# Optimization experiments

Measured on AMD Instinct MI355X. Metric: run time of the kernel, lower is better.

## Reference

```python
import jax, jax.numpy as jnp
from jax import lax
import numpy as np

HH = WW = 128          # backbone feature map (2048px image / stride 16)
C_IN = 512
FEAT_STRIDE = 16
N_ANCHOR = 9
NMS_THRESH = 0.7
N_PRE_NMS = 6000
N_POST_NMS = 300
MIN_SIZE = 16
NEG = jnp.float32(-1e30)


def _anchor_base(base_size=16, ratios=(0.5, 1.0, 2.0), scales=(8, 16, 32)):
    py = px = base_size / 2.0
    ab = np.zeros((len(ratios) * len(scales), 4), np.float32)
    for i, r in enumerate(ratios):
        for j, s in enumerate(scales):
            h = base_size * s * np.sqrt(r)
            w = base_size * s * np.sqrt(1.0 / r)
            ab[i * len(scales) + j] = [py - h / 2, px - w / 2, py + h / 2, px + w / 2]
    return ab


def _shifted_anchors(hh, ww):
    # (y1, x1, y2, x2) anchors enumerated row-major over (y, x), anchors innermost
    ab = _anchor_base()
    sy = np.arange(0, hh * FEAT_STRIDE, FEAT_STRIDE, dtype=np.float32)
    sx = np.arange(0, ww * FEAT_STRIDE, FEAT_STRIDE, dtype=np.float32)
    sx, sy = np.meshgrid(sx, sy)
    shift = np.stack((sy.ravel(), sx.ravel(), sy.ravel(), sx.ravel()), axis=1)
    anc = (ab[None, :, :] + shift[:, None, :]).reshape(-1, 4)
    return jnp.asarray(anc)


def _conv(x, w, b):
    y = lax.conv_general_dilated(x, w, (1, 1), 'SAME',
                                 dimension_numbers=('NHWC', 'HWIO', 'NHWC'))
    return y + b


def _loc2bbox(anchor, loc):
    sh = anchor[:, 2] - anchor[:, 0]
    sw = anchor[:, 3] - anchor[:, 1]
    scy = anchor[:, 0] + 0.5 * sh
    scx = anchor[:, 1] + 0.5 * sw
    cy = loc[:, 0] * sh + scy
    cx = loc[:, 1] * sw + scx
    h = jnp.exp(loc[:, 2]) * sh
    w = jnp.exp(loc[:, 3]) * sw
    return jnp.stack([cy - 0.5 * h, cx - 0.5 * w, cy + 0.5 * h, cx + 0.5 * w], axis=1)


def _nms(boxes, scores, thresh, n_out):
    # Greedy NMS with a fixed output size; invalid slots are zeroed.
    y1, x1, y2, x2 = boxes[:, 0], boxes[:, 1], boxes[:, 2], boxes[:, 3]
    areas = (y2 - y1) * (x2 - x1)

    def step(valid, _):
        s = jnp.where(valid, scores, NEG)
        i = jnp.argmax(s)
        ok = s[i] > NEG
        iy1 = jnp.maximum(y1, y1[i]); ix1 = jnp.maximum(x1, x1[i])
        iy2 = jnp.minimum(y2, y2[i]); ix2 = jnp.minimum(x2, x2[i])
        inter = jnp.maximum(iy2 - iy1, 0.0) * jnp.maximum(ix2 - ix1, 0.0)
        iou = inter / (areas + areas[i] - inter + 1e-9)
        valid = valid & (iou <= thresh)  # picked box suppresses itself (iou=1)
        return valid, (i, ok)

    _, (idx, oks) = lax.scan(step, jnp.ones(scores.shape, bool), None, length=n_out)
    return boxes[idx] * oks[:, None].astype(boxes.dtype)


def _proposals(loc, fg_score, anchor, img_h, img_w, scale):
    dst = _loc2bbox(anchor, loc)
    dst = jnp.stack([jnp.clip(dst[:, 0], 0.0, img_h),
                     jnp.clip(dst[:, 1], 0.0, img_w),
                     jnp.clip(dst[:, 2], 0.0, img_h),
                     jnp.clip(dst[:, 3], 0.0, img_w)], axis=1)
    min_size = MIN_SIZE * scale
    hs = dst[:, 2] - dst[:, 0]
    ws = dst[:, 3] - dst[:, 1]
    keep = (hs >= min_size) & (ws >= min_size)
    sc = jnp.where(keep, fg_score, -jnp.inf)
    top_s, top_i = lax.top_k(sc, N_PRE_NMS)
    return _nms(dst[top_i], top_s, NMS_THRESH, N_POST_NMS)


def _rpn_forward(x, conv_w, conv_b, loc_w, loc_b, score_w, score_b, img_h, img_w, scale):
    n, hh, ww, _ = x.shape
    anchor = _shifted_anchors(hh, ww)                    # [hh*ww*9, 4]
    h = jax.nn.relu(_conv(x, conv_w, conv_b))            # [n, hh, ww, 512]
    rpn_loc = _conv(h, loc_w, loc_b).reshape(n, -1, 4)   # [n, hh*ww*9, 4]
    rpn_score_map = _conv(h, score_w, score_b)           # [n, hh, ww, 18]
    soft = jax.nn.softmax(rpn_score_map.reshape(n, hh, ww, N_ANCHOR, 2), axis=-1)
    rpn_fg = soft[..., 1].reshape(n, -1)                 # [n, hh*ww*9]
    rpn_score = rpn_score_map.reshape(n, -1, 2)
    roi = _proposals(rpn_loc[0], rpn_fg[0], anchor, img_h, img_w, scale)  # [300, 4]
    return rpn_loc, rpn_score, roi, anchor


def setup_inputs() -> dict:
    key = jax.random.key(0)
    ks = jax.random.split(key, 4)
    return {
        "x": jax.random.normal(ks[0], (1, HH, WW, C_IN), jnp.float32),
        "conv_w": jax.random.normal(ks[1], (3, 3, C_IN, 512), jnp.float32) * 0.02,
        "conv_b": jnp.zeros((512,), jnp.float32),
        "loc_w": jax.random.normal(ks[2], (1, 1, 512, 36), jnp.float32) * 0.02,
        "loc_b": jnp.zeros((36,), jnp.float32),
        "score_w": jax.random.normal(ks[3], (1, 1, 512, 18), jnp.float32) * 0.02,
        "score_b": jnp.zeros((18,), jnp.float32),
        "img_h": HH * FEAT_STRIDE,
        "img_w": WW * FEAT_STRIDE,
        "scale": 1,
    }


def reference(x, conv_w, conv_b, loc_w, loc_b, score_w, score_b, img_h, img_w, scale):
    return _rpn_forward(x, conv_w, conv_b, loc_w, loc_b, score_w, score_b,
                        float(img_h), float(img_w), float(scale))
```

## Files before the change

kernel.cpp:

```cpp
#include <hip/hip_runtime.h>
#include <math.h>

typedef unsigned int u32;
typedef unsigned long long u64;
typedef _Float16 half8 __attribute__((ext_vector_type(8)));
typedef float f32x4 __attribute__((ext_vector_type(4)));
typedef float f32x16 __attribute__((ext_vector_type(16)));

#define N_PIX 16384
#define N_ANC 147456
#define N_PRE 6000
#define TIE_BASE 6144
#define TIE_CAP  16384

#define OFF_H      0ULL
#define OFF_BOXES  33554432ULL
#define OFF_KEYS   35913728ULL
#define OFF_W54    36503552ULL
#define OFF_B54    36634624ULL
#define OFF_HIST1  36634880ULL
#define OFF_HIST2  36897024ULL
#define OFF_CTRL   37159168ULL
#define OFF_CAND   37159424ULL
#define OFF_SBOX   37339648ULL
#define OFF_MASK   37437952ULL
#define BASE_NEEDED 41961984ULL
#define OFF_XH     41961984ULL
#define OFF_XL     58739200ULL
#define OFF_WHT    75516416ULL
#define OFF_WLT    80235008ULL
#define FULL_NEEDED 84953600ULL

#define KEY_NEGINF 0x007FFFFFu

#define MASK_BYTES 4524032ULL

struct AB { float v[36]; };


__device__ __forceinline__ void d_init_body(int i0, u32* hist1, u32* hist2, u32* ctrl, float* roi,
                       float* w54, float* b54,
                       const float* __restrict__ loc_w, const float* __restrict__ loc_b,
                       const float* __restrict__ score_w, const float* __restrict__ score_b) {
  const int stride = 256 * 256;
  const int TOT = 65536 * 2 + 64 + 1200 + 32768 + 64;
  for (int i = i0; i < TOT; i += stride) {
    if (i < 65536) hist1[i] = 0u;
    else if (i < 131072) hist2[i - 65536] = 0u;
    else if (i < 131136) ctrl[i - 131072] = 0u;
    else if (i < 132336) roi[i - 131136] = 0.f;
    else if (i < 165104) {
      int j = i - 132336;
      int k = j >> 6, oc = j & 63;
      float v = 0.f;
      if (oc < 36) v = loc_w[k * 36 + oc];
      else if (oc < 54) v = score_w[k * 18 + oc - 36];
      w54[(((k >> 2) << 6) + oc) * 4 + (k & 3)] = v;
    } else {
      int oc = i - 165104;
      float v = 0.f;
      if (oc < 36) v = loc_b[oc];
      else if (oc < 54) v = score_b[oc - 36];
      b54[oc] = v;
    }
  }
}

__device__ __forceinline__ void d_split_x_body(int b, int t, const float* __restrict__ x,
                                               _Float16* __restrict__ xh, _Float16* __restrict__ xl) {
  const int gid = b * 256 + t;
  const int base = gid << 3;
  float a[8];
  *(float4*)&a[0] = *(const float4*)(x + base);
  *(float4*)&a[4] = *(const float4*)(x + base + 4);
  half8 hh, ll;
#pragma unroll
  for (int j = 0; j < 8; ++j) {
    _Float16 hi = (_Float16)a[j];
    hh[j] = hi;
    ll[j] = (_Float16)((a[j] - (float)hi) * 2048.0f);
  }
  *(half8*)(xh + base) = hh;
  *(half8*)(xl + base) = ll;
}

__device__ __forceinline__ void d_split_w_body(int kb, int cb, int t, const float* __restrict__ w,
                                               _Float16* __restrict__ whT, _Float16* __restrict__ wlT,
                                               _Float16 (*th)[72], _Float16 (*tl)[72]) {
  {
    const int r = t >> 2, cq = t & 3;
    float a[16];
    const float* wp = w + ((size_t)(kb * 64 + r) << 9) + cb * 64 + cq * 16;
#pragma unroll
    for (int j = 0; j < 4; ++j) *(float4*)&a[j << 2] = *(const float4*)(wp + (j << 2));
    half8 h0, h1, l0, l1;
#pragma unroll
    for (int j = 0; j < 8; ++j) {
      _Float16 hi = (_Float16)a[j];
      h0[j] = hi; l0[j] = (_Float16)((a[j] - (float)hi) * 2048.0f);
    }
#pragma unroll
    for (int j = 0; j < 8; ++j) {
      _Float16 hi = (_Float16)a[8 + j];
      h1[j] = hi; l1[j] = (_Float16)((a[8 + j] - (float)hi) * 2048.0f);
    }
    *(half8*)&th[r][cq * 16]     = h0;
    *(half8*)&th[r][cq * 16 + 8] = h1;
    *(half8*)&tl[r][cq * 16]     = l0;
    *(half8*)&tl[r][cq * 16 + 8] = l1;
  }
  __syncthreads();
  {
    const int c = t >> 2, kq = t & 3;
    half8 o0, o1, p0, p1;
#pragma unroll
    for (int j = 0; j < 8; ++j) { o0[j] = th[kq * 16 + j][c];     p0[j] = tl[kq * 16 + j][c]; }
#pragma unroll
    for (int j = 0; j < 8; ++j) { o1[j] = th[kq * 16 + 8 + j][c]; p1[j] = tl[kq * 16 + 8 + j][c]; }
    const size_t dst = (size_t)(cb * 64 + c) * 4608 + kb * 64 + kq * 16;
    *(half8*)(whT + dst)     = o0;
    *(half8*)(whT + dst + 8) = o1;
    *(half8*)(wlT + dst)     = p0;
    *(half8*)(wlT + dst + 8) = p1;
  }
}

__global__ void k_init(u32* hist1, u32* hist2, u32* ctrl, float* roi,
                       float* w54, float* b54,
                       const float* __restrict__ loc_w, const float* __restrict__ loc_b,
                       const float* __restrict__ score_w, const float* __restrict__ score_b) {
  const int i0 = blockIdx.x * blockDim.x + threadIdx.x;
  d_init_body(i0, hist1, hist2, ctrl, roi, w54, b54, loc_w, loc_b, score_w, score_b);
}

__global__ __launch_bounds__(256) void k_prep(const float* __restrict__ x,
                                              _Float16* __restrict__ xh, _Float16* __restrict__ xl,
                                              const float* __restrict__ w,
                                              _Float16* __restrict__ whT, _Float16* __restrict__ wlT,
                                              u32* hist1, u32* hist2, u32* ctrl, float* roi,
                                              float* w54, float* b54,
                                              const float* __restrict__ loc_w, const float* __restrict__ loc_b,
                                              const float* __restrict__ score_w, const float* __restrict__ score_b) {
  __shared__ _Float16 th[64][72];
  __shared__ _Float16 tl[64][72];
  const int b = blockIdx.x;
  const int t = threadIdx.x;
  if (b < 4096) {
    d_split_x_body(b, t, x, xh, xl);
  } else if (b < 4672) {
    const int idx = b - 4096;
    d_split_w_body(idx % 72, idx / 72, t, w, whT, wlT, th, tl);
  } else {
    d_init_body((b - 4672) * 256 + t, hist1, hist2, ctrl, roi, w54, b54, loc_w, loc_b, score_w, score_b);
  }
}

__global__ __launch_bounds__(256, 2) void k_conv_pre(const _Float16* __restrict__ xh,
                                                     const _Float16* __restrict__ xl,
                                                     const _Float16* __restrict__ whT,
                                                     const _Float16* __restrict__ wlT,
                                                     const float* __restrict__ bias,
                                                     float* __restrict__ h) {
  __shared__ _Float16 As[2][2][4][128][8];
  __shared__ _Float16 Bs[2][2][4][128][8];

  const int bid = blockIdx.x;
  const int q   = bid >> 3;
  const int nb  = q >> 4;
  const int y   = ((bid & 7) << 4) + (q & 15);

  const int t  = threadIdx.x;
  const int wv = t >> 6, lane = t & 63;
  const int m0 = (wv >> 1) << 6;
  const int n0 = (wv & 1) << 6;
  const int ln5 = lane & 31;
  const int kh  = lane >> 5;

  const int s_m = t >> 1;
  const int kq0 = (t & 1) << 1;
  const int ch0 = kq0 << 3;

  f32x16 acc_hh[2][2];
  f32x16 acc_x[2][2];
#pragma unroll
  for (int i = 0; i < 2; ++i)
#pragma unroll
    for (int j = 0; j < 2; ++j) { acc_hh[i][j] = (f32x16)0.f; acc_x[i][j] = (f32x16)0.f; }

  const int ct0 = (s_m - 1) << 9;
  const int ct1 = s_m << 9;
  const int ct2 = (s_m + 1) << 9;
  const bool cok0 = (s_m >= 1);
  const bool cok2 = (s_m <= 126);
  const u32 bb = (u32)(nb * 128 + s_m) * 4608u + (u32)ch0;

  half8 rah0, rah1, ral0, ral1, rbh0, rbh1, rbl0, rbl1;

#define CONV_LOAD(KB)                                                            \
  {                                                                              \
    const int ci_   = (KB) / 9;                           \
    const int tap_  = (KB) - ci_ * 9;                        \
    const int ky_   = tap_ / 3, kx_ = tap_ - ky_ * 3;                            \
    const int cin0_ = ci_ << 5;                                                  \
    const int yy_   = y + ky_ - 1;                                               \
    const bool rok_ = (yy_ >= 0) && (yy_ < 128);                                 \
    const int colterm_ = (kx_ == 0) ? ct0 : ((kx_ == 1) ? ct1 : ct2);            \
    const bool cok_    = (kx_ == 0) ? cok0 : ((kx_ == 1) ? true : cok2);         \
    if (rok_ && cok_) {                                                          \
      const u32 aoff_ = (u32)((yy_ << 16) + cin0_ + ch0 + colterm_);             \
      rah0 = *(const half8*)(xh + aoff_);                                        \
      rah1 = *(const half8*)(xh + aoff_ + 8);                                    \
      ral0 = *(const half8*)(xl + aoff_);                                        \
      ral1 = *(const half8*)(xl + aoff_ + 8);                                    \
    } else {                                                                     \
      rah0 = (half8)(_Float16)0; rah1 = (half8)(_Float16)0;                      \
      ral0 = (half8)(_Float16)0; ral1 = (half8)(_Float16)0;                      \
    }                                                                            \
    const u32 boff_ = bb + (u32)(tap_ * 512 + cin0_);                            \
    rbh0 = *(const half8*)(whT + boff_);                                         \
    rbh1 = *(const half8*)(whT + boff_ + 8);                                     \
    rbl0 = *(const half8*)(wlT + boff_);                                         \
    rbl1 = *(const half8*)(wlT + boff_ + 8);                                     \
  }

#define CONV_STORE(BUF)                                                          \
  {                                                                              \
    *(half8*)As[BUF][0][kq0][s_m]     = rah0;                                    \
    *(half8*)As[BUF][0][kq0 + 1][s_m] = rah1;                                    \
    *(half8*)As[BUF][1][kq0][s_m]     = ral0;                                    \
    *(half8*)As[BUF][1][kq0 + 1][s_m] = ral1;                                    \
    *(half8*)Bs[BUF][0][kq0][s_m]     = rbh0;                                    \
    *(half8*)Bs[BUF][0][kq0 + 1][s_m] = rbh1;                                    \
    *(half8*)Bs[BUF][1][kq0][s_m]     = rbl0;                                    \
    *(half8*)Bs[BUF][1][kq0 + 1][s_m] = rbl1;                                    \
  }

#define FRAGS(KS, AH, AL, BH, BL)                                                \
  {                                                                              \
    const int kq_ = ((KS) << 1) + kh;                                            \
    _Pragma("unroll")                                                            \
    for (int i = 0; i < 2; ++i) {                                                \
      AH[i] = *(const half8*)As[cur][0][kq_][m0 + (i << 5) + ln5];               \
      AL[i] = *(const half8*)As[cur][1][kq_][m0 + (i << 5) + ln5];               \
      BH[i] = *(const half8*)Bs[cur][0][kq_][n0 + (i << 5) + ln5];               \
      BL[i] = *(const half8*)Bs[cur][1][kq_][n0 + (i << 5) + ln5];               \
    }                                                                            \
  }

#define MFMA12(AH, AL, BH, BL)                                                   \
  {                                                                              \
    _Pragma("unroll")                                                            \
    for (int mi = 0; mi < 2; ++mi)                                               \
      _Pragma("unroll")                                                          \
      for (int ni = 0; ni < 2; ++ni) {                                           \
        acc_hh[mi][ni] = __builtin_amdgcn_mfma_f32_32x32x16_f16(AH[mi], BH[ni], acc_hh[mi][ni], 0, 0, 0); \
        acc_x[mi][ni]  = __builtin_amdgcn_mfma_f32_32x32x16_f16(AH[mi], BL[ni], acc_x[mi][ni], 0, 0, 0);  \
        acc_x[mi][ni]  = __builtin_amdgcn_mfma_f32_32x32x16_f16(AL[mi], BH[ni], acc_x[mi][ni], 0, 0, 0);  \
      }                                                                          \
  }

  CONV_LOAD(0);
  CONV_STORE(0);
  __syncthreads();

  int cur = 0;
#pragma unroll 1
  for (int kb = 0; kb < 143; ++kb) {
    half8 a0h[2], a0l[2], b0h[2], b0l[2];
    FRAGS(0, a0h, a0l, b0h, b0l);
    CONV_LOAD(kb + 1);
    __builtin_amdgcn_sched_barrier(0);
    __builtin_amdgcn_s_setprio(1);
    MFMA12(a0h, a0l, b0h, b0l);
    __builtin_amdgcn_s_setprio(0);
    half8 a1h[2], a1l[2], b1h[2], b1l[2];
    FRAGS(1, a1h, a1l, b1h, b1l);
    __builtin_amdgcn_s_setprio(1);
    MFMA12(a1h, a1l, b1h, b1l);
    __builtin_amdgcn_s_setprio(0);
    CONV_STORE(cur ^ 1);
    __syncthreads();
    cur ^= 1;
  }
  {
    half8 a0h[2], a0l[2], b0h[2], b0l[2];
    FRAGS(0, a0h, a0l, b0h, b0l);
    MFMA12(a0h, a0l, b0h, b0l);
    half8 a1h[2], a1l[2], b1h[2], b1l[2];
    FRAGS(1, a1h, a1l, b1h, b1l);
    MFMA12(a1h, a1l, b1h, b1l);
  }
#undef CONV_LOAD
#undef CONV_STORE
#undef FRAGS
#undef MFMA12

  const float inv2048 = 1.0f / 2048.0f;
#pragma unroll
  for (int mi = 0; mi < 2; ++mi)
#pragma unroll
    for (int ni = 0; ni < 2; ++ni) {
      const int col = n0 + (ni << 5) + ln5;
      const float bbv = bias[(nb << 7) + col];
#pragma unroll
      for (int r = 0; r < 16; ++r) {
        const int row = m0 + (mi << 5) + (r & 3) + ((r >> 2) << 3) + (kh << 2);
        float v = acc_hh[mi][ni][r] + acc_x[mi][ni][r] * inv2048 + bbv;
        h[(((size_t)((y << 7) + row)) << 9) + (nb << 7) + col] = fmaxf(v, 0.f);
      }
    }
}

#define APAD 40
__global__ __launch_bounds__(256, 2) void k_conv_fb(const float* __restrict__ x,
                                                    const float* __restrict__ w,
                                                    const float* __restrict__ bias,
                                                    float* __restrict__ h) {
  __shared__ _Float16 Ah[128][APAD];
  __shared__ _Float16 Al[128][APAD];
  __shared__ _Float16 Bh[128][APAD];
  __shared__ _Float16 Bl[128][APAD];

  const int y  = blockIdx.x;
  const int nb = blockIdx.y;
  const int t  = threadIdx.x;
  const int wv = t >> 6, lane = t & 63;
  const int m0 = (wv >> 1) << 6;
  const int n0 = (wv & 1) << 6;
  const int fm = lane & 15;
  const int fq = lane >> 4;
  const int sa_m = t >> 1;
  const int sa_h = (t & 1) << 4;
  const int sb_n = t & 127;
  const int sb_kg = (t >> 7) << 4;

  f32x4 acc_hh[4][4];
  f32x4 acc_x[4][4];
#pragma unroll
  for (int i = 0; i < 4; ++i)
#pragma unroll
    for (int j = 0; j < 4; ++j) { acc_hh[i][j] = (f32x4)0.f; acc_x[i][j] = (f32x4)0.f; }

#pragma unroll 1
  for (int kb = 0; kb < 144; ++kb) {
    const int tap  = kb >> 4;
    const int ky   = tap / 3, kx = tap - ky * 3;
    const int cin0 = (kb & 15) << 5;
    {
      const int yy = y + ky - 1;
      const int xx = sa_m + kx - 1;
      float av[16];
      if (yy >= 0 && yy < 128 && xx >= 0 && xx < 128) {
        const float* ap = x + (((size_t)((yy << 7) + xx)) << 9) + cin0 + sa_h;
#pragma unroll
        for (int j = 0; j < 4; ++j) *(float4*)&av[j << 2] = *(const float4*)(ap + (j << 2));
      } else {
#pragma unroll
        for (int j = 0; j < 16; ++j) av[j] = 0.f;
      }
      half8 h0, h1, l0, l1;
#pragma unroll
      for (int j = 0; j < 8; ++j) {
        _Float16 hi = (_Float16)av[j];
        h0[j] = hi; l0[j] = (_Float16)((av[j] - (float)hi) * 2048.0f);
      }
#pragma unroll
      for (int j = 0; j < 8; ++j) {
        _Float16 hi = (_Float16)av[8 + j];
        h1[j] = hi; l1[j] = (_Float16)((av[8 + j] - (float)hi) * 2048.0f);
      }
      *(half8*)&Ah[sa_m][sa_h]     = h0;
      *(half8*)&Ah[sa_m][sa_h + 8] = h1;
      *(half8*)&Al[sa_m][sa_h]     = l0;
      *(half8*)&Al[sa_m][sa_h + 8] = l1;
    }
    {
      const float* bp = w + ((size_t)(tap * 512 + cin0 + sb_kg) << 9) + (nb << 7) + sb_n;
      float bv[16];
#pragma unroll
      for (int j = 0; j < 16; ++j) bv[j] = bp[(size_t)j << 9];
      half8 h0, h1, l0, l1;
#pragma unroll
      for (int j = 0; j < 8; ++j) {
        _Float16 hi = (_Float16)bv[j];
        h0[j] = hi; l0[j] = (_Float16)((bv[j] - (float)hi) * 2048.0f);
      }
#pragma unroll
      for (int j = 0; j < 8; ++j) {
        _Float16 hi = (_Float16)bv[8 + j];
        h1[j] = hi; l1[j] = (_Float16)((bv[8 + j] - (float)hi) * 2048.0f);
      }
      *(half8*)&Bh[sb_n][sb_kg]     = h0;
      *(half8*)&Bh[sb_n][sb_kg + 8] = h1;
      *(half8*)&Bl[sb_n][sb_kg]     = l0;
      *(half8*)&Bl[sb_n][sb_kg + 8] = l1;
    }
    __syncthreads();
    half8 ah[4], al[4], bh[4], bl[4];
#pragma unroll
    for (int i = 0; i < 4; ++i) {
      ah[i] = *(const half8*)&Ah[m0 + (i << 4) + fm][fq << 3];
      al[i] = *(const half8*)&Al[m0 + (i << 4) + fm][fq << 3];
      bh[i] = *(const half8*)&Bh[n0 + (i << 4) + fm][fq << 3];
      bl[i] = *(const half8*)&Bl[n0 + (i << 4) + fm][fq << 3];
    }
#pragma unroll
    for (int mi = 0; mi < 4; ++mi)
#pragma unroll
      for (int ni = 0; ni < 4; ++ni) {
        acc_hh[mi][ni] = __builtin_amdgcn_mfma_f32_16x16x32_f16(ah[mi], bh[ni], acc_hh[mi][ni], 0, 0, 0);
        acc_x[mi][ni]  = __builtin_amdgcn_mfma_f32_16x16x32_f16(ah[mi], bl[ni], acc_x[mi][ni], 0, 0, 0);
        acc_x[mi][ni]  = __builtin_amdgcn_mfma_f32_16x16x32_f16(al[mi], bh[ni], acc_x[mi][ni], 0, 0, 0);
      }
    __syncthreads();
  }
  const float inv2048 = 1.0f / 2048.0f;
#pragma unroll
  for (int mi = 0; mi < 4; ++mi)
#pragma unroll
    for (int ni = 0; ni < 4; ++ni) {
      const int col = n0 + (ni << 4) + fm;
      const float bb = bias[(nb << 7) + col];
#pragma unroll
      for (int r = 0; r < 4; ++r) {
        const int row = m0 + (mi << 4) + (fq << 2) + r;
        float v = acc_hh[mi][ni][r] + acc_x[mi][ni][r] * inv2048 + bb;
        h[(((size_t)((y << 7) + row)) << 9) + (nb << 7) + col] = fmaxf(v, 0.f);
      }
    }
}

__global__ __launch_bounds__(256) void k_heads(const float* __restrict__ h,
        const float4* __restrict__ w54, const float* __restrict__ b54,
        float* __restrict__ out0, float* __restrict__ out1, float* __restrict__ out3,
        float4* __restrict__ boxes, u32* __restrict__ keys, u32* __restrict__ hist1,
        const int* __restrict__ p_ih, const int* __restrict__ p_iw,
        const int* __restrict__ p_sc, AB ab) {
  __shared__ float hl[16 * 512];
  __shared__ float vals[16][64];
  const int t = threadIdx.x;
  const int wv = t >> 6, lane = t & 63;
  const int pbase = blockIdx.x << 4;

#pragma unroll
  for (int j = 0; j < 8; ++j) {
    const int f = (j << 8) + t;
    ((float4*)hl)[f] = ((const float4*)(h + ((size_t)pbase << 9)))[f];
  }
  __syncthreads();

  const float* hp = hl + ((wv << 2) << 9);
  float a0 = 0.f, a1 = 0.f, a2 = 0.f, a3 = 0.f;
#pragma unroll 4
  for (int kq = 0; kq < 128; ++kq) {
    const float4 wvv = w54[(kq << 6) + lane];
    const float4 h0 = *(const float4*)(hp + (kq << 2));
    const float4 h1 = *(const float4*)(hp + 512 + (kq << 2));
    const float4 h2 = *(const float4*)(hp + 1024 + (kq << 2));
    const float4 h3 = *(const float4*)(hp + 1536 + (kq << 2));
    a0 += h0.x * wvv.x + h0.y * wvv.y + h0.z * wvv.z + h0.w * wvv.w;
    a1 += h1.x * wvv.x + h1.y * wvv.y + h1.z * wvv.z + h1.w * wvv.w;
    a2 += h2.x * wvv.x + h2.y * wvv.y + h2.z * wvv.z + h2.w * wvv.w;
    a3 += h3.x * wvv.x + h3.y * wvv.y + h3.z * wvv.z + h3.w * wvv.w;
  }
  const float bb = b54[lane];
  float av[4] = {a0 + bb, a1 + bb, a2 + bb, a3 + bb};
#pragma unroll
  for (int px = 0; px < 4; ++px) {
    const int p = pbase + (wv << 2) + px;
    vals[(wv << 2) + px][lane] = av[px];
    if (lane < 36) out0[p * 36 + lane] = av[px];
    else if (lane < 54) out1[p * 18 + lane - 36] = av[px];
  }
  __syncthreads();

  if (lane < 36) {
    const int px = lane / 9, a = lane - px * 9;
    const int p = pbase + (wv << 2) + px;
    const float* vv = vals[(wv << 2) + px];
    const float l0 = vv[(a << 2) + 0], l1 = vv[(a << 2) + 1];
    const float l2 = vv[(a << 2) + 2], l3 = vv[(a << 2) + 3];
    const float s0 = vv[36 + (a << 1)], s1 = vv[37 + (a << 1)];
    const int yq = p >> 7, xq = p & 127;
    const float fy = (float)(yq << 4), fx = (float)(xq << 4);
    const float ay1 = ab.v[(a << 2) + 0] + fy;
    const float ax1 = ab.v[(a << 2) + 1] + fx;
    const float ay2 = ab.v[(a << 2) + 2] + fy;
    const float ax2 = ab.v[(a << 2) + 3] + fx;
    const int idx = p * 9 + a;
    *(float4*)(out3 + ((size_t)idx << 2)) = make_float4(ay1, ax1, ay2, ax2);

    const float sh = ay2 - ay1, sw = ax2 - ax1;
    const float scy = ay1 + 0.5f * sh, scx = ax1 + 0.5f * sw;
    const float cy = l0 * sh + scy, cx = l1 * sw + scx;
    const float bh = expf(l2) * sh, bw = expf(l3) * sw;
    const float IH = (float)p_ih[0], IW = (float)p_iw[0];
    float d0 = fminf(fmaxf(cy - 0.5f * bh, 0.f), IH);
    float d1 = fminf(fmaxf(cx - 0.5f * bw, 0.f), IW);
    float d2 = fminf(fmaxf(cy + 0.5f * bh, 0.f), IH);
    float d3 = fminf(fmaxf(cx + 0.5f * bw, 0.f), IW);
    boxes[idx] = make_float4(d0, d1, d2, d3);

    const float minsz = 16.f * (float)p_sc[0];
    const bool keep = (d2 - d0 >= minsz) && (d3 - d1 >= minsz);
    const float mx = fmaxf(s0, s1);
    const float e0 = expf(s0 - mx), e1 = expf(s1 - mx);
    const float fg = e1 / (e0 + e1);
    const float sc = keep ? fg : -INFINITY;
    const u32 u = __float_as_uint(sc);
    const u32 key = (u & 0x80000000u) ? ~u : (u | 0x80000000u);
    keys[idx] = key;
    atomicAdd(&hist1[key >> 16], 1u);
  }
}

__global__ void k_hist2(const u32* __restrict__ keys, const u32* __restrict__ ctrl,
                        u32* __restrict__ hist2) {
  const u32 b1 = ctrl[0];
  int i = blockIdx.x * blockDim.x + threadIdx.x;
  if (i < N_ANC) {
    const u32 k = keys[i];
    if ((k >> 16) == b1) atomicAdd(&hist2[k & 0xFFFFu], 1u);
  }
}

__global__ __launch_bounds__(1024) void k_findcut(const u32* __restrict__ hist,
                                                  u32* __restrict__ ctrl, int mode) {
  __shared__ u32 csum[1024];
  __shared__ u32 suf[1024];
  const int t = threadIdx.x;
  const u32 target = (mode == 0) ? (u32)N_PRE : ((u32)N_PRE - ctrl[1]);
  const int base = t << 6;
  u32 s = 0;
  for (int i = 0; i < 64; ++i) s += hist[base + i];
  csum[t] = s;
  suf[t] = s;
  __syncthreads();
  for (int off = 1; off < 1024; off <<= 1) {
    u32 add = (t + off < 1024) ? suf[t + off] : 0u;
    __syncthreads();
    suf[t] += add;
    __syncthreads();
  }
  const u32 excl = suf[t] - csum[t];
  if (excl < target && target <= suf[t]) {
    u32 cum = excl;
    int bkt = base;
    for (int i = 63; i >= 0; --i) {
      const u32 hh = hist[base + i];
      if (cum < target && target <= cum + hh) { bkt = base + i; break; }
      cum += hh;
    }
    if (mode == 0) { ctrl[0] = (u32)bkt; ctrl[1] = cum; }
    else {
      const u32 Kstar = (ctrl[0] << 16) | (u32)bkt;
      const u32 A = ctrl[1] + cum;
      u32 need = (u32)N_PRE - A;
      if (Kstar == KEY_NEGINF) need = 0u;
      ctrl[2] = Kstar; ctrl[3] = A; ctrl[4] = need;
      ctrl[7] = A + need;
    }
  }
}

__global__ void k_compact(const u32* __restrict__ keys, u32* __restrict__ ctrl,
                          u64* __restrict__ cand) {
  const u32 Kstar = ctrl[2];
  const u32 need  = ctrl[4];
  int i = blockIdx.x * blockDim.x + threadIdx.x;
  if (i >= N_ANC) return;
  const u32 k = keys[i];
  if (k > Kstar) {
    const u32 pos = atomicAdd(&ctrl[5], 1u);
    cand[pos] = ((u64)k << 32) | (u64)(u32)(~(u32)i);
  } else if (k == Kstar && need != 0u) {
    const u32 pos = atomicAdd(&ctrl[6], 1u);
    if (pos < (u32)TIE_CAP) cand[TIE_BASE + pos] = ((u64)Kstar << 32) | (u64)(u32)(~(u32)i);
  }
}

__global__ __launch_bounds__(128) void k_rank(const u32* __restrict__ ctrl,
                                              const u64* __restrict__ cand,
                                              const float4* __restrict__ boxes,
                                              float4* __restrict__ sbox) {
  __shared__ u32 wred[2];
  const u32 A   = ctrl[3];
  const u32 tcc = min(ctrl[6], (u32)TIE_CAP);
  const u32 C   = A + tcc;
  const u32 L   = ctrl[7];
  const int t   = threadIdx.x;
  for (u32 i = blockIdx.x; i < C; i += gridDim.x) {
    const u64 v = (i < A) ? cand[i] : cand[TIE_BASE + (i - A)];
    u32 cnt = 0;
    for (u32 j = t; j < A; j += 128) cnt += (cand[j] > v);
    for (u32 j = t; j < tcc; j += 128) cnt += (cand[TIE_BASE + j] > v);
#pragma unroll
    for (int off = 32; off > 0; off >>= 1) cnt += __shfl_xor(cnt, off);
    if ((t & 63) == 0) wred[t >> 6] = cnt;
    __syncthreads();
    if (t == 0) {
      const u32 rank = wred[0] + wred[1];
      if (rank < L) {
        const u32 idx = ~((u32)(v & 0xFFFFFFFFULL));
        sbox[rank] = boxes[idx];
      }
    }
    __syncthreads();
  }
}

__global__ __launch_bounds__(256) void k_mask(const u32* __restrict__ ctrl,
                                              const float4* __restrict__ sbox,
                                              u64* __restrict__ mask) {
  const int L = (int)ctrl[7];
  const int rb = blockIdx.y;
  if (rb * 64 >= L) return;
  const int wv = threadIdx.x >> 6;
  const int lane = threadIdx.x & 63;
  const int cw = (blockIdx.x << 2) + wv;
  if (cw > 93 || cw < rb) return;
  const int j = cw * 64 + lane;
  const bool jok = (j < L);
  const float4 cb = jok ? sbox[j] : make_float4(0.f, 0.f, 0.f, 0.f);
  const float careaJ = (cb.z - cb.x) * (cb.w - cb.y);
  const int rbase = rb * 64;
  const float4 rbx = (rbase + lane < L) ? sbox[rbase + lane] : make_float4(0.f, 0.f, 0.f, 0.f);
  const int rmax = min(64, L - rbase);
  for (int r = 0; r < rmax; ++r) {
    const float ry1 = __shfl(rbx.x, r), rx1 = __shfl(rbx.y, r);
    const float ry2 = __shfl(rbx.z, r), rx2 = __shfl(rbx.w, r);
    const float ra = (ry2 - ry1) * (rx2 - rx1);
    const float iy1 = fmaxf(cb.x, ry1), ix1 = fmaxf(cb.y, rx1);
    const float iy2 = fminf(cb.z, ry2), ix2 = fminf(cb.w, rx2);
    const float inter = fmaxf(iy2 - iy1, 0.f) * fmaxf(ix2 - ix1, 0.f);
    const float iou = inter / (careaJ + ra - inter + 1e-9f);
    const bool bit = jok && (iou > 0.7f);
    const u64 bal = __ballot(bit);
    if (lane == 0) mask[(size_t)(rbase + r) * 94 + cw] = bal;
  }
}

__device__ inline u64 valid_mask_fn(int base, int L) {
  const int r = L - base;
  if (r <= 0) return 0ULL;
  if (r >= 64) return ~0ULL;
  return (1ULL << r) - 1ULL;
}
__device__ inline u64 above_mask_fn(int base, int i) {
  if (i < base) return ~0ULL;
  const int s = i - base + 1;
  if (s >= 64) return 0ULL;
  return (~0ULL) << s;
}

__device__ __forceinline__ void gload_lds16(const void* g, void* l) {
  __builtin_amdgcn_global_load_lds(
      (const __attribute__((address_space(1))) void*)g,
      (__attribute__((address_space(3))) void*)l, 16, 0, 0);
}

__global__ __launch_bounds__(64) void k_greedy(const u32* __restrict__ ctrl,
                                               const float* __restrict__ sboxf,
                                               const u64* __restrict__ mask,
                                               float* __restrict__ roi) {
  __shared__ char lds[4 * 12288];
  const int lane = threadIdx.x;
  const int L = (int)ctrl[7];
  if (L <= 0) return;
  const char* gmask = (const char*)mask;
  const char* gend  = gmask + MASK_BYTES;
  const int nbatch = (L + 15) >> 4;

#define GISSUE(BB)                                                         \
  {                                                                        \
    const char* gb_ = gmask + (size_t)(BB) * 12032;                        \
    char* lb_ = lds + ((BB) & 3) * 12288;                                  \
    _Pragma("unroll")                                                      \
    for (int j_ = 0; j_ < 12; ++j_) {                                      \
      const char* ga_ = gb_ + j_ * 1024;                                   \
      if (ga_ + 1024 > gend) ga_ = gend - 1024;    \
      gload_lds16(ga_ + lane * 16, lb_ + j_ * 1024);                       \
    }                                                                      \
  }

  int issued = 0;
  for (; issued < nbatch && issued < 4; ++issued) GISSUE(issued);

  const int base0 = lane << 6;
  const int base1 = (64 + lane) << 6;
  const u64 v0 = valid_mask_fn(base0, L);
  const u64 v1 = (lane < 30) ? valid_mask_fn(base1, L) : 0ULL;
  u64 rem0 = 0ULL, rem1 = 0ULL;
  int i = 0, kept = 0;

  for (int b = 0; b < nbatch && i >= 0 && kept < 300; ++b) {
    const int out = issued - b - 1;
    if (out >= 3)      asm volatile("s_waitcnt vmcnt(36)" ::: "memory");
    else if (out == 2) asm volatile("s_waitcnt vmcnt(24)" ::: "memory");
    else if (out == 1) asm volatile("s_waitcnt vmcnt(12)" ::: "memory");
    else               asm volatile("s_waitcnt vmcnt(0)"  ::: "memory");
    const int hi = (b + 1) << 4;
    while (i >= 0 && i < hi && kept < 300) {
      if (lane < 4) roi[kept * 4 + lane] = sboxf[(size_t)i * 4 + lane];
      ++kept;
      const u64* rowp = (const u64*)(lds + (((u32)i >> 4) & 3) * 12288 + (i & 15) * 752);
      rem0 |= rowp[lane];
      if (lane < 30) rem1 |= rowp[64 + lane];
      const u64 f0 = ~rem0 & v0 & above_mask_fn(base0, i);
      const u64 f1 = ~rem1 & v1 & above_mask_fn(base1, i);
      int c0 = f0 ? (base0 + (int)__builtin_ctzll(f0)) : 0x7FFFFFFF;
      int c1 = f1 ? (base1 + (int)__builtin_ctzll(f1)) : 0x7FFFFFFF;
      int c = min(c0, c1);
#pragma unroll
      for (int off = 1; off < 64; off <<= 1) c = min(c, __shfl_xor(c, off));
      i = (c == 0x7FFFFFFF) ? -1 : c;
    }
    if (issued < nbatch) { GISSUE(issued); ++issued; }
  }
#undef GISSUE
}

extern "C" void kernel_launch(void* const* d_in, const int* in_sizes, int n_in,
                              void* d_out, int out_size, void* d_ws, size_t ws_size,
                              hipStream_t stream) {
  (void)in_sizes; (void)n_in; (void)out_size;
  if (ws_size < BASE_NEEDED) return;
  const bool fast = (ws_size >= FULL_NEEDED);

  const float* x       = (const float*)d_in[0];
  const float* conv_w  = (const float*)d_in[1];
  const float* conv_b  = (const float*)d_in[2];
  const float* loc_w   = (const float*)d_in[3];
  const float* loc_b   = (const float*)d_in[4];
  const float* score_w = (const float*)d_in[5];
  const float* score_b = (const float*)d_in[6];
  const int* p_ih = (const int*)d_in[7];
  const int* p_iw = (const int*)d_in[8];
  const int* p_sc = (const int*)d_in[9];

  float* out0 = (float*)d_out;
  float* out1 = out0 + 589824;
  float* roi  = out1 + 294912;
  float* out3 = roi + 1200;

  char* ws = (char*)d_ws;
  float*     h     = (float*)(ws + OFF_H);
  float4*    boxes = (float4*)(ws + OFF_BOXES);
  u32*       keys  = (u32*)(ws + OFF_KEYS);
  float*     w54   = (float*)(ws + OFF_W54);
  float*     b54   = (float*)(ws + OFF_B54);
  u32*       hist1 = (u32*)(ws + OFF_HIST1);
  u32*       hist2 = (u32*)(ws + OFF_HIST2);
  u32*       ctrl  = (u32*)(ws + OFF_CTRL);
  u64*       cand  = (u64*)(ws + OFF_CAND);
  float4*    sbox  = (float4*)(ws + OFF_SBOX);
  u64*       mask  = (u64*)(ws + OFF_MASK);
  _Float16*  xh    = (_Float16*)(ws + OFF_XH);
  _Float16*  xl    = (_Float16*)(ws + OFF_XL);
  _Float16*  whT   = (_Float16*)(ws + OFF_WHT);
  _Float16*  wlT   = (_Float16*)(ws + OFF_WLT);

  AB ab;
  {
    const double ratios[3] = {0.5, 1.0, 2.0};
    const double scales[3] = {8.0, 16.0, 32.0};
    for (int i = 0; i < 3; ++i)
      for (int j = 0; j < 3; ++j) {
        const double hh = 16.0 * scales[j] * sqrt(ratios[i]);
        const double wwv = 16.0 * scales[j] * sqrt(1.0 / ratios[i]);
        const int a = i * 3 + j;
        ab.v[a * 4 + 0] = (float)(8.0 - hh / 2.0);
        ab.v[a * 4 + 1] = (float)(8.0 - wwv / 2.0);
        ab.v[a * 4 + 2] = (float)(8.0 + hh / 2.0);
        ab.v[a * 4 + 3] = (float)(8.0 + wwv / 2.0);
      }
  }

  if (fast) {
    hipLaunchKernelGGL(k_prep, dim3(4928), dim3(256), 0, stream,
                       x, xh, xl, conv_w, whT, wlT,
                       hist1, hist2, ctrl, roi, w54, b54, loc_w, loc_b, score_w, score_b);
    hipLaunchKernelGGL(k_conv_pre, dim3(512), dim3(256), 0, stream, xh, xl, whT, wlT, conv_b, h);
  } else {
    hipLaunchKernelGGL(k_init, dim3(256), dim3(256), 0, stream,
                       hist1, hist2, ctrl, roi, w54, b54, loc_w, loc_b, score_w, score_b);
    hipLaunchKernelGGL(k_conv_fb, dim3(128, 4), dim3(256), 0, stream, x, conv_w, conv_b, h);
  }
  hipLaunchKernelGGL(k_heads, dim3(1024), dim3(256), 0, stream,
                     h, (const float4*)w54, b54, out0, out1, out3, boxes, keys, hist1,
                     p_ih, p_iw, p_sc, ab);
  hipLaunchKernelGGL(k_findcut, dim3(1), dim3(1024), 0, stream, hist1, ctrl, 0);
  hipLaunchKernelGGL(k_hist2, dim3(576), dim3(256), 0, stream, keys, ctrl, hist2);
  hipLaunchKernelGGL(k_findcut, dim3(1), dim3(1024), 0, stream, hist2, ctrl, 1);
  hipLaunchKernelGGL(k_compact, dim3(576), dim3(256), 0, stream, keys, ctrl, cand);
  hipLaunchKernelGGL(k_rank, dim3(8192), dim3(128), 0, stream, ctrl, cand, boxes, sbox);
  hipLaunchKernelGGL(k_mask, dim3(24, 94), dim3(256), 0, stream, ctrl, sbox, mask);
  hipLaunchKernelGGL(k_greedy, dim3(1), dim3(64), 0, stream, ctrl, (const float*)sbox, mask, roi);
}
```

Before: 717.6 us.

## Load conv weights directly into registers and skip NMS batches via ballot search

The conv GEMM no longer stages weight tiles through LDS. Each wave now loads its B fragments straight from global memory into registers, double-buffered across an unrolled-by-two K loop, which halves LDS traffic and shared memory use. The risk is more global loads per wave, since fragments are no longer shared across waves, plus higher register pressure. Separately, the NMS scan replaces the shuffle-reduction minimum with a ballot plus ctz search, and jumps directly to the batch holding the next surviving box, issuing prefetches on demand instead of walking every batch in order.

```diff
diff --git a/kernel.cpp b/kernel.cpp
--- a/kernel.cpp
+++ b/kernel.cpp
@@ -162,7 +162,6 @@
                                                      const float* __restrict__ bias,
                                                      float* __restrict__ h) {
   __shared__ _Float16 As[2][2][4][128][8];
-  __shared__ _Float16 Bs[2][2][4][128][8];
 
   const int bid = blockIdx.x;
   const int q   = bid >> 3;
@@ -192,14 +191,16 @@
   const int ct2 = (s_m + 1) << 9;
   const bool cok0 = (s_m >= 1);
   const bool cok2 = (s_m <= 126);
-  const u32 bb = (u32)(nb * 128 + s_m) * 4608u + (u32)ch0;
-
-  half8 rah0, rah1, ral0, ral1, rbh0, rbh1, rbl0, rbl1;
-
-#define CONV_LOAD(KB)                                                            \
+
+  const u32 wrow0 = (u32)(nb * 128 + n0 + ln5) * 4608u + (u32)(kh << 3);
+
+  half8 rah0, rah1, ral0, ral1;
+  half8 bh0[2][2], bl0[2][2], bh1[2][2], bl1[2][2];
+
+#define CONV_LOADA(KB)                                                           \
   {                                                                              \
-    const int ci_   = (KB) / 9;                           \
-    const int tap_  = (KB) - ci_ * 9;                        \
+    const int ci_   = (KB) / 9;                                                  \
+    const int tap_  = (KB) - ci_ * 9;                                            \
     const int ky_   = tap_ / 3, kx_ = tap_ - ky_ * 3;                            \
     const int cin0_ = ci_ << 5;                                                  \
     const int yy_   = y + ky_ - 1;                                               \
@@ -216,84 +217,106 @@
       rah0 = (half8)(_Float16)0; rah1 = (half8)(_Float16)0;                      \
       ral0 = (half8)(_Float16)0; ral1 = (half8)(_Float16)0;                      \
     }                                                                            \
-    const u32 boff_ = bb + (u32)(tap_ * 512 + cin0_);                            \
-    rbh0 = *(const half8*)(whT + boff_);                                         \
-    rbh1 = *(const half8*)(whT + boff_ + 8);                                     \
-    rbl0 = *(const half8*)(wlT + boff_);                                         \
-    rbl1 = *(const half8*)(wlT + boff_ + 8);                                     \
-  }
-
-#define CONV_STORE(BUF)                                                          \
+  }
+
+#define CONV_STOREA(BUF)                                                         \
   {                                                                              \
     *(half8*)As[BUF][0][kq0][s_m]     = rah0;                                    \
     *(half8*)As[BUF][0][kq0 + 1][s_m] = rah1;                                    \
     *(half8*)As[BUF][1][kq0][s_m]     = ral0;                                    \
     *(half8*)As[BUF][1][kq0 + 1][s_m] = ral1;                                    \
-    *(half8*)Bs[BUF][0][kq0][s_m]     = rbh0;                                    \
-    *(half8*)Bs[BUF][0][kq0 + 1][s_m] = rbh1;                                    \
-    *(half8*)Bs[BUF][1][kq0][s_m]     = rbl0;                                    \
-    *(half8*)Bs[BUF][1][kq0 + 1][s_m] = rbl1;                                    \
-  }
-
-#define FRAGS(KS, AH, AL, BH, BL)                                                \
+  }
+
+#define BLOAD(KB, BH, BL)                                                        \
+  {                                                                              \
+    const int ci_  = (KB) / 9;                                                   \
+    const int tap_ = (KB) - ci_ * 9;                                             \
+    const u32 koff_ = (u32)(tap_ * 512 + (ci_ << 5));                            \
+    _Pragma("unroll")                                                            \
+    for (int i_ = 0; i_ < 2; ++i_) {                                             \
+      _Pragma("unroll")                                                          \
+      for (int ks_ = 0; ks_ < 2; ++ks_) {                                        \
+        const u32 o_ = wrow0 + (u32)i_ * 147456u + koff_ + ((u32)ks_ << 4);      \
+        BH[i_][ks_] = *(const half8*)(whT + o_);                                 \
+        BL[i_][ks_] = *(const half8*)(wlT + o_);                                 \
+      }                                                                          \
+    }                                                                            \
+  }
+
+#define FRAGSA(KS, AH, AL)                                                       \
   {                                                                              \
     const int kq_ = ((KS) << 1) + kh;                                            \
     _Pragma("unroll")                                                            \
     for (int i = 0; i < 2; ++i) {                                                \
       AH[i] = *(const half8*)As[cur][0][kq_][m0 + (i << 5) + ln5];               \
       AL[i] = *(const half8*)As[cur][1][kq_][m0 + (i << 5) + ln5];               \
-      BH[i] = *(const half8*)Bs[cur][0][kq_][n0 + (i << 5) + ln5];               \
-      BL[i] = *(const half8*)Bs[cur][1][kq_][n0 + (i << 5) + ln5];               \
     }                                                                            \
   }
 
-#define MFMA12(AH, AL, BH, BL)                                                   \
+#define MFMA6(AH, AL, BH, BL, KS)                                                \
   {                                                                              \
     _Pragma("unroll")                                                            \
     for (int mi = 0; mi < 2; ++mi)                                               \
       _Pragma("unroll")                                                          \
       for (int ni = 0; ni < 2; ++ni) {                                           \
-        acc_hh[mi][ni] = __builtin_amdgcn_mfma_f32_32x32x16_f16(AH[mi], BH[ni], acc_hh[mi][ni], 0, 0, 0); \
-        acc_x[mi][ni]  = __builtin_amdgcn_mfma_f32_32x32x16_f16(AH[mi], BL[ni], acc_x[mi][ni], 0, 0, 0);  \
-        acc_x[mi][ni]  = __builtin_amdgcn_mfma_f32_32x32x16_f16(AL[mi], BH[ni], acc_x[mi][ni], 0, 0, 0);  \
+        acc_hh[mi][ni] = __builtin_amdgcn_mfma_f32_32x32x16_f16(AH[mi], BH[ni][KS], acc_hh[mi][ni], 0, 0, 0); \
+        acc_x[mi][ni]  = __builtin_amdgcn_mfma_f32_32x32x16_f16(AH[mi], BL[ni][KS], acc_x[mi][ni], 0, 0, 0);  \
+        acc_x[mi][ni]  = __builtin_amdgcn_mfma_f32_32x32x16_f16(AL[mi], BH[ni][KS], acc_x[mi][ni], 0, 0, 0);  \
       }                                                                          \
   }
 
-  CONV_LOAD(0);
-  CONV_STORE(0);
+  CONV_LOADA(0);
+  BLOAD(0, bh0, bl0);
+  CONV_STOREA(0);
   __syncthreads();
 
   int cur = 0;
 #pragma unroll 1
-  for (int kb = 0; kb < 143; ++kb) {
-    half8 a0h[2], a0l[2], b0h[2], b0l[2];
-    FRAGS(0, a0h, a0l, b0h, b0l);
-    CONV_LOAD(kb + 1);
-    __builtin_amdgcn_sched_barrier(0);
-    __builtin_amdgcn_s_setprio(1);
-    MFMA12(a0h, a0l, b0h, b0l);
-    __builtin_amdgcn_s_setprio(0);
-    half8 a1h[2], a1l[2], b1h[2], b1l[2];
-    FRAGS(1, a1h, a1l, b1h, b1l);
-    __builtin_amdgcn_s_setprio(1);
-    MFMA12(a1h, a1l, b1h, b1l);
-    __builtin_amdgcn_s_setprio(0);
-    CONV_STORE(cur ^ 1);
-    __syncthreads();
-    cur ^= 1;
-  }
-  {
-    half8 a0h[2], a0l[2], b0h[2], b0l[2];
-    FRAGS(0, a0h, a0l, b0h, b0l);
-    MFMA12(a0h, a0l, b0h, b0l);
-    half8 a1h[2], a1l[2], b1h[2], b1l[2];
-    FRAGS(1, a1h, a1l, b1h, b1l);
-    MFMA12(a1h, a1l, b1h, b1l);
-  }
-#undef CONV_LOAD
-#undef CONV_STORE
-#undef FRAGS
-#undef MFMA12
+  for (int kb = 0; kb < 144; kb += 2) {
+    {
+      half8 a0h[2], a0l[2], a1h[2], a1l[2];
+      FRAGSA(0, a0h, a0l);
+      CONV_LOADA(kb + 1);
+      BLOAD(kb + 1, bh1, bl1);
+      __builtin_amdgcn_sched_barrier(0);
+      __builtin_amdgcn_s_setprio(1);
+      MFMA6(a0h, a0l, bh0, bl0, 0);
+      __builtin_amdgcn_s_setprio(0);
+      FRAGSA(1, a1h, a1l);
+      __builtin_amdgcn_s_setprio(1);
+      MFMA6(a1h, a1l, bh0, bl0, 1);
+      __builtin_amdgcn_s_setprio(0);
+      CONV_STOREA(cur ^ 1);
+      __syncthreads();
+      cur ^= 1;
+    }
+    {
+      half8 a0h[2], a0l[2], a1h[2], a1l[2];
+      FRAGSA(0, a0h, a0l);
+      if (kb + 2 < 144) {
+        CONV_LOADA(kb + 2);
+        BLOAD(kb + 2, bh0, bl0);
+      }
+      __builtin_amdgcn_sched_barrier(0);
+      __builtin_amdgcn_s_setprio(1);
+      MFMA6(a0h, a0l, bh1, bl1, 0);
+      __builtin_amdgcn_s_setprio(0);
+      FRAGSA(1, a1h, a1l);
+      __builtin_amdgcn_s_setprio(1);
+      MFMA6(a1h, a1l, bh1, bl1, 1);
+      __builtin_amdgcn_s_setprio(0);
+      if (kb + 2 < 144) {
+        CONV_STOREA(cur ^ 1);
+        __syncthreads();
+        cur ^= 1;
+      }
+    }
+  }
+#undef CONV_LOADA
+#undef CONV_STOREA
+#undef BLOAD
+#undef FRAGSA
+#undef MFMA6
 
   const float inv2048 = 1.0f / 2048.0f;
 #pragma unroll
@@ -683,9 +706,8 @@
     }                                                                      \
   }
 
-  int issued = 0;
-  for (; issued < nbatch && issued < 4; ++issued) GISSUE(issued);
-
+  int next_issue = 0;
+  int ready = -1;
   const int base0 = lane << 6;
   const int base1 = (64 + lane) << 6;
   const u64 v0 = valid_mask_fn(base0, L);
@@ -693,29 +715,41 @@
   u64 rem0 = 0ULL, rem1 = 0ULL;
   int i = 0, kept = 0;
 
-  for (int b = 0; b < nbatch && i >= 0 && kept < 300; ++b) {
-    const int out = issued - b - 1;
-    if (out >= 3)      asm volatile("s_waitcnt vmcnt(36)" ::: "memory");
-    else if (out == 2) asm volatile("s_waitcnt vmcnt(24)" ::: "memory");
-    else if (out == 1) asm volatile("s_waitcnt vmcnt(12)" ::: "memory");
-    else               asm volatile("s_waitcnt vmcnt(0)"  ::: "memory");
-    const int hi = (b + 1) << 4;
-    while (i >= 0 && i < hi && kept < 300) {
-      if (lane < 4) roi[kept * 4 + lane] = sboxf[(size_t)i * 4 + lane];
-      ++kept;
-      const u64* rowp = (const u64*)(lds + (((u32)i >> 4) & 3) * 12288 + (i & 15) * 752);
-      rem0 |= rowp[lane];
-      if (lane < 30) rem1 |= rowp[64 + lane];
-      const u64 f0 = ~rem0 & v0 & above_mask_fn(base0, i);
-      const u64 f1 = ~rem1 & v1 & above_mask_fn(base1, i);
-      int c0 = f0 ? (base0 + (int)__builtin_ctzll(f0)) : 0x7FFFFFFF;
-      int c1 = f1 ? (base1 + (int)__builtin_ctzll(f1)) : 0x7FFFFFFF;
-      int c = min(c0, c1);
-#pragma unroll
-      for (int off = 1; off < 64; off <<= 1) c = min(c, __shfl_xor(c, off));
-      i = (c == 0x7FFFFFFF) ? -1 : c;
-    }
-    if (issued < nbatch) { GISSUE(issued); ++issued; }
+  while (i >= 0 && kept < 300) {
+    const int bi = i >> 4;
+    if (bi > ready) {
+      if (next_issue < bi) next_issue = bi;
+      const int want = min(bi + 3, nbatch - 1);
+      while (next_issue <= want) { GISSUE(next_issue); ++next_issue; }
+      const int out = next_issue - 1 - bi;
+      if (out >= 3)      asm volatile("s_waitcnt vmcnt(36)" ::: "memory");
+      else if (out == 2) asm volatile("s_waitcnt vmcnt(24)" ::: "memory");
+      else if (out == 1) asm volatile("s_waitcnt vmcnt(12)" ::: "memory");
+      else               asm volatile("s_waitcnt vmcnt(0)"  ::: "memory");
+      ready = bi;
+    }
+    if (lane < 4) roi[kept * 4 + lane] = sboxf[(size_t)i * 4 + lane];
+    ++kept;
+    const u64* rowp = (const u64*)(lds + (bi & 3) * 12288 + (i & 15) * 752);
+    rem0 |= rowp[lane];
+    if (lane < 30) rem1 |= rowp[64 + lane];
+    const u64 f0 = ~rem0 & v0 & above_mask_fn(base0, i);
+    const u64 f1 = ~rem1 & v1 & above_mask_fn(base1, i);
+    int ni = -1;
+    const u64 b0 = __ballot(f0 != 0ULL);
+    if (b0) {
+      const int w = (int)__builtin_ctzll(b0);
+      const u64 fw = (u64)__shfl((long long)f0, w);
+      ni = (w << 6) + (int)__builtin_ctzll(fw);
+    } else {
+      const u64 b1m = __ballot(f1 != 0ULL);
+      if (b1m) {
+        const int w = (int)__builtin_ctzll(b1m);
+        const u64 fw = (u64)__shfl((long long)f1, w);
+        ni = ((64 + w) << 6) + (int)__builtin_ctzll(fw);
+      }
+    }
+    i = ni;
   }
 #undef GISSUE
 }
```

Result: slower. 782.9 us (+9.1%).
